# Performance work log

Measured on AMD Instinct MI355X. Metric: run time of the kernel, lower is better.

The kernel has to match this reference:

```python
import jax, jax.numpy as jnp
import numpy as np
import math

N_HEAD = 8

def setup_inputs() -> dict:
    key = jax.random.key(0)
    ks = jax.random.split(key, 5)
    B, T, D = 1, 4096, 512
    x = jax.random.normal(ks[0], (B, T, D), dtype=jnp.float32)
    s = 0.02
    Wq = jax.random.normal(ks[1], (D, D), dtype=jnp.float32) * s
    Wk = jax.random.normal(ks[2], (D, D), dtype=jnp.float32) * s
    Wv = jax.random.normal(ks[3], (D, D), dtype=jnp.float32) * s
    Wo = jax.random.normal(ks[4], (D, D), dtype=jnp.float32) * s
    return {"x": x, "Wq": Wq, "Wk": Wk, "Wv": Wv, "Wo": Wo, "window": 64}

def reference(x, Wq, Wk, Wv, Wo, window):
    # SparseAttention with attend_fn = causal sliding window of size `window`.
    # key_indices[q] = [max(0, q-window+1) .. q]
    B, T, D = x.shape
    H = N_HEAD
    Dh = D // H
    scale = math.sqrt(Dh)
    # torch Linear(bias=False): y = x @ W.T
    Q = (x @ Wq.T).reshape(B, T, H, Dh)
    K = (x @ Wk.T).reshape(B, T, H, Dh)
    V = (x @ Wv.T).reshape(B, T, H, Dh)
    # per-query gather indices [T, w] with validity mask (honors sparsity;
    # never materializes a [T, T] score matrix)
    offs = jnp.arange(window) - (window - 1)          # [-w+1 .. 0]
    idx = jnp.arange(T)[:, None] + offs[None, :]       # [T, w]
    valid = idx >= 0                                   # [T, w]
    idx_c = jnp.clip(idx, 0, T - 1)
    Kg = K[:, idx_c]                                   # [B, T, w, H, Dh]
    Vg = V[:, idx_c]                                   # [B, T, w, H, Dh]
    scores = jnp.einsum('bthd,btwhd->bhtw', Q, Kg) / scale
    scores = jnp.where(valid[None, None, :, :], scores, jnp.finfo(scores.dtype).min)
    attn = jax.nn.softmax(scores, axis=-1)             # dropout=0.0 (eval)
    out = jnp.einsum('bhtw,btwhd->bthd', attn, Vg).reshape(B, T, D)
    return out @ Wo.T
```

## Files before the change

kernel.cpp:

```cpp
#include <hip/hip_runtime.h>
#include <hip/hip_bf16.h>
#include <math.h>


typedef __attribute__((ext_vector_type(8))) short bf16frag;
typedef __attribute__((ext_vector_type(4))) float f32x4;
typedef __attribute__((ext_vector_type(8))) unsigned short u16x8;

#if defined(__has_builtin)
#if __has_builtin(__builtin_amdgcn_global_load_lds)
#define HAVE_GLOAD_LDS 1
#endif
#endif

__device__ inline void gload16(const void* g, void* l, int lane) {
#ifdef HAVE_GLOAD_LDS
    __builtin_amdgcn_global_load_lds(
        (const __attribute__((address_space(1))) void*)g,
        (__attribute__((address_space(3))) void*)l, 16, 0, 0);
#else
    *(bf16frag*)((char*)l + lane * 16) = *(const bf16frag*)g;
#endif
}

__device__ inline unsigned short bf16_rne(float f) {
    unsigned int u = __float_as_uint(f);
    unsigned int r = u + 0x7fffu + ((u >> 16) & 1u);
    return (unsigned short)(r >> 16);
}

__device__ inline void split_val(float f, unsigned short& h, unsigned short& l) {
    h = bf16_rne(f);
    float hf = __uint_as_float(((unsigned int)h) << 16);
    float lf = f - hf;
    l = bf16_rne(lf);
}

__global__ __launch_bounds__(256) void split5(
    const float* __restrict__ x, const float* __restrict__ wq, const float* __restrict__ wk,
    const float* __restrict__ wv, const float* __restrict__ wo,
    unsigned short* xh, unsigned short* xl, unsigned short* qh, unsigned short* ql,
    unsigned short* kh, unsigned short* kl, unsigned short* vh, unsigned short* vl,
    unsigned short* oh, unsigned short* ol, int nx, int nw)
{
    const float* src; unsigned short *H, *L; int n;
    switch (blockIdx.z) {
        case 0: src = x;  H = xh; L = xl; n = nx; break;
        case 1: src = wq; H = qh; L = ql; n = nw; break;
        case 2: src = wk; H = kh; L = kl; n = nw; break;
        case 3: src = wv; H = vh; L = vl; n = nw; break;
        default: src = wo; H = oh; L = ol; n = nw; break;
    }
    int stride = gridDim.x * blockDim.x * 4;
    for (int i = (blockIdx.x * blockDim.x + threadIdx.x) * 4; i < n; i += stride) {
        float4 f = *(const float4*)(src + i);
        ushort4 h4, l4;
        split_val(f.x, h4.x, l4.x);
        split_val(f.y, h4.y, l4.y);
        split_val(f.z, h4.z, l4.z);
        split_val(f.w, h4.w, l4.w);
        *(ushort4*)(H + i) = h4;
        *(ushort4*)(L + i) = l4;
    }
}

__global__ __launch_bounds__(256) void zero_pad(
    unsigned short* __restrict__ VTH, unsigned short* __restrict__ VTL, int vtw)
{
    int i = blockIdx.x * blockDim.x + threadIdx.x;
    if (i < 512 * 63) {
        int r = i / 63, c = i % 63;
        VTH[(size_t)r * vtw + c] = 0;
        VTL[(size_t)r * vtw + c] = 0;
    }
}

template<int BM, int MODE>
__global__ __launch_bounds__(256) void gemm_lds(
    const unsigned short* __restrict__ Ah, const unsigned short* __restrict__ Al,
    const unsigned short* __restrict__ W0h, const unsigned short* __restrict__ W0l,
    const unsigned short* __restrict__ W1h, const unsigned short* __restrict__ W1l,
    const unsigned short* __restrict__ W2h, const unsigned short* __restrict__ W2l,
    float* __restrict__ C0, float* __restrict__ C1, float* __restrict__ C2,
    unsigned short* __restrict__ QHo, unsigned short* __restrict__ QLo,
    unsigned short* __restrict__ KHo, unsigned short* __restrict__ KLo,
    unsigned short* __restrict__ VTHo, unsigned short* __restrict__ VTLo, int vtw)
{
    constexpr int MT     = BM / 32;
    constexpr int HALF   = BM / 2;
    constexpr int ABYTES = BM * 128;
    constexpr int NINST  = (BM + 64) * 128 / 1024;
    constexpr int PER_WAVE = NINST / 4;

    __shared__ unsigned char lds[(BM + 64) * 128];

    const unsigned short *Wh, *Wl;
    if (blockIdx.z == 0)      { Wh = W0h; Wl = W0l; }
    else if (blockIdx.z == 1) { Wh = W1h; Wl = W1l; }
    else                      { Wh = W2h; Wl = W2l; }

    const int tid  = threadIdx.x;
    const int wid  = tid >> 6;
    const int lane = tid & 63;
    const int wr = wid >> 1, wc = wid & 1;
    const int m0 = blockIdx.y * BM;
    const int n0 = blockIdx.x * 64;

    f32x4 acc[MT][2];
    #pragma unroll
    for (int i = 0; i < MT; ++i) {
        acc[i][0] = (f32x4){0.f, 0.f, 0.f, 0.f};
        acc[i][1] = (f32x4){0.f, 0.f, 0.f, 0.f};
    }

    for (int ks = 0; ks < 24; ++ks) {
        const int rg = ks >> 3;
        const int k0 = (ks & 7) << 6;
        const unsigned short* As = (rg < 2) ? Ah : Al;
        const unsigned short* Bs = (rg == 1) ? Wl : Wh;

        __syncthreads();
        #pragma unroll
        for (int j = 0; j < PER_WAVE; ++j) {
            const int o  = (wid * PER_WAVE + j) << 10;
            const int li = o + lane * 16;
            const void* g;
            if (li < ABYTES) {
                const int r  = li >> 7;
                const int kb = (li & 127) ^ ((r & 7) << 4);
                g = As + (size_t)(m0 + r) * 512 + k0 + (kb >> 1);
            } else {
                const int lb = li - ABYTES;
                const int r  = lb >> 7;
                const int kb = (lb & 127) ^ ((r & 7) << 4);
                g = Bs + (size_t)(n0 + r) * 512 + k0 + (kb >> 1);
            }
            gload16(g, lds + o, lane);
        }
        __syncthreads();

        #pragma unroll
        for (int ksub = 0; ksub < 2; ++ksub) {
            const int kbb = (ksub << 6) + ((lane >> 4) << 4);
            bf16frag af[MT], bf[2];
            #pragma unroll
            for (int mt = 0; mt < MT; ++mt) {
                const int r = wr * HALF + mt * 16 + (lane & 15);
                af[mt] = *(const bf16frag*)(lds + r * 128 + (kbb ^ ((r & 7) << 4)));
            }
            #pragma unroll
            for (int nt = 0; nt < 2; ++nt) {
                const int r = wc * 32 + nt * 16 + (lane & 15);
                bf[nt] = *(const bf16frag*)(lds + ABYTES + r * 128 + (kbb ^ ((r & 7) << 4)));
            }
            #pragma unroll
            for (int mt = 0; mt < MT; ++mt)
                #pragma unroll
                for (int nt = 0; nt < 2; ++nt)
                    acc[mt][nt] = __builtin_amdgcn_mfma_f32_16x16x32_bf16(
                        af[mt], bf[nt], acc[mt][nt], 0, 0, 0);
        }
    }

    const int rbase = (lane >> 4) * 4;
    #pragma unroll
    for (int mt = 0; mt < MT; ++mt)
        #pragma unroll
        for (int nt = 0; nt < 2; ++nt) {
            const int col = n0 + wc * 32 + nt * 16 + (lane & 15);
            #pragma unroll
            for (int j = 0; j < 4; ++j) {
                const int row = m0 + wr * HALF + mt * 16 + rbase + j;
                if constexpr (MODE == 0) {
                    float* C = (blockIdx.z == 0) ? C0 : (blockIdx.z == 1 ? C1 : C2);
                    C[(size_t)row * 512 + col] = acc[mt][nt][j];
                } else {
                    unsigned short hh, ll;
                    split_val(acc[mt][nt][j], hh, ll);
                    if (blockIdx.z == 0) {
                        QHo[(size_t)row * 512 + col] = hh;
                        QLo[(size_t)row * 512 + col] = ll;
                    } else if (blockIdx.z == 1) {
                        KHo[(size_t)row * 512 + col] = hh;
                        KLo[(size_t)row * 512 + col] = ll;
                    } else {
                        VTHo[(size_t)col * vtw + 63 + row] = hh;
                        VTLo[(size_t)col * vtw + 63 + row] = ll;
                    }
                }
            }
        }
}

__global__ __launch_bounds__(128) void swattn5(
    const unsigned short* __restrict__ QH, const unsigned short* __restrict__ QL,
    const unsigned short* __restrict__ KH, const unsigned short* __restrict__ KL,
    const unsigned short* __restrict__ VTH, const unsigned short* __restrict__ VTL,
    unsigned short* __restrict__ OH, unsigned short* __restrict__ OL, int T)
{
    __shared__ unsigned short KsH[96 * 88], KsL[96 * 88];
    __shared__ unsigned short VtH[64 * 104], VtL[64 * 104];
    __shared__ unsigned short PsH[32 * 104], PsL[32 * 104];

    const int h   = blockIdx.x & 7;
    const int t0  = (blockIdx.x >> 3) * 32;
    const int kt0 = t0 - 63;
    const int tid = threadIdx.x;
    const int vtw = T + 64;

    {
        const int c = tid & 7;
        for (int r = tid >> 3; r < 96; r += 16) {
            const int kt = kt0 + r;
            u16x8 kh = {0,0,0,0,0,0,0,0}, kl = {0,0,0,0,0,0,0,0};
            if (kt >= 0 && r < 95) {
                const size_t off = (size_t)kt * 512 + h * 64 + c * 8;
                kh = *(const u16x8*)(KH + off);
                kl = *(const u16x8*)(KL + off);
            }
            *(u16x8*)&KsH[r * 88 + c * 8] = kh;
            *(u16x8*)&KsL[r * 88 + c * 8] = kl;
        }
    }
    for (int i = tid; i < 64 * 12; i += 128) {
        const int d = i / 12, c = i % 12;
        const size_t off = (size_t)(h * 64 + d) * vtw + t0 + c * 8;
        *(u16x8*)&VtH[d * 104 + c * 8] = *(const u16x8*)(VTH + off);
        *(u16x8*)&VtL[d * 104 + c * 8] = *(const u16x8*)(VTL + off);
    }
    __syncthreads();

    const int wid  = tid >> 6;
    const int lane = tid & 63;
    const int lr = lane & 15;
    const int lg = lane >> 4;

    bf16frag qfh[2], qfl[2];
    {
        const size_t base = (size_t)(t0 + wid * 16 + lr) * 512 + h * 64 + lg * 8;
        qfh[0] = *(const bf16frag*)(QH + base);
        qfh[1] = *(const bf16frag*)(QH + base + 32);
        qfl[0] = *(const bf16frag*)(QL + base);
        qfl[1] = *(const bf16frag*)(QL + base + 32);
    }

    f32x4 s[6];
    #pragma unroll
    for (int wt = 0; wt < 6; ++wt) s[wt] = (f32x4){0.f, 0.f, 0.f, 0.f};
    #pragma unroll
    for (int ksub = 0; ksub < 2; ++ksub) {
        #pragma unroll
        for (int wt = 0; wt < 6; ++wt) {
            const int a = (wt * 16 + lr) * 88 + lg * 8 + ksub * 32;
            bf16frag akh = *(const bf16frag*)&KsH[a];
            bf16frag akl = *(const bf16frag*)&KsL[a];
            s[wt] = __builtin_amdgcn_mfma_f32_16x16x32_bf16(akh, qfh[ksub], s[wt], 0, 0, 0);
            s[wt] = __builtin_amdgcn_mfma_f32_16x16x32_bf16(akh, qfl[ksub], s[wt], 0, 0, 0);
            s[wt] = __builtin_amdgcn_mfma_f32_16x16x32_bf16(akl, qfh[ksub], s[wt], 0, 0, 0);
        }
    }

    const int q_local = wid * 16 + lr;
    float sc[6][4];
    float mx = -3e38f;
    #pragma unroll
    for (int wt = 0; wt < 6; ++wt)
        #pragma unroll
        for (int j = 0; j < 4; ++j) {
            const int w = wt * 16 + lg * 4 + j;
            const bool valid = (w >= q_local) && (w <= q_local + 63) && (kt0 + w >= 0);
            sc[wt][j] = valid ? s[wt][j] * 0.125f : -3e38f;
            mx = fmaxf(mx, sc[wt][j]);
        }
    mx = fmaxf(mx, __shfl_xor(mx, 16));
    mx = fmaxf(mx, __shfl_xor(mx, 32));
    float sum = 0.f;
    #pragma unroll
    for (int wt = 0; wt < 6; ++wt)
        #pragma unroll
        for (int j = 0; j < 4; ++j) {
            sc[wt][j] = __expf(sc[wt][j] - mx);
            sum += sc[wt][j];
        }
    sum += __shfl_xor(sum, 16);
    sum += __shfl_xor(sum, 32);
    const float inv = 1.f / sum;

    #pragma unroll
    for (int wt = 0; wt < 6; ++wt) {
        ushort4 ph, pl;
        unsigned short hh, ll;
        split_val(sc[wt][0] * inv, hh, ll); ph.x = hh; pl.x = ll;
        split_val(sc[wt][1] * inv, hh, ll); ph.y = hh; pl.y = ll;
        split_val(sc[wt][2] * inv, hh, ll); ph.z = hh; pl.z = ll;
        split_val(sc[wt][3] * inv, hh, ll); ph.w = hh; pl.w = ll;
        const int col = wt * 16 + lg * 4;
        *(ushort4*)&PsH[q_local * 104 + col] = ph;
        *(ushort4*)&PsL[q_local * 104 + col] = pl;
    }

    f32x4 oa[4];
    #pragma unroll
    for (int dt = 0; dt < 4; ++dt) oa[dt] = (f32x4){0.f, 0.f, 0.f, 0.f};
    #pragma unroll
    for (int ks = 0; ks < 3; ++ks) {
        const int ka = lg * 8 + ks * 32;
        bf16frag pah = *(const bf16frag*)&PsH[(wid * 16 + lr) * 104 + ka];
        bf16frag pal = *(const bf16frag*)&PsL[(wid * 16 + lr) * 104 + ka];
        #pragma unroll
        for (int dt = 0; dt < 4; ++dt) {
            const int a = (dt * 16 + lr) * 104 + ka;
            bf16frag bvh = *(const bf16frag*)&VtH[a];
            bf16frag bvl = *(const bf16frag*)&VtL[a];
            oa[dt] = __builtin_amdgcn_mfma_f32_16x16x32_bf16(pah, bvh, oa[dt], 0, 0, 0);
            oa[dt] = __builtin_amdgcn_mfma_f32_16x16x32_bf16(pal, bvh, oa[dt], 0, 0, 0);
            oa[dt] = __builtin_amdgcn_mfma_f32_16x16x32_bf16(pah, bvl, oa[dt], 0, 0, 0);
        }
    }

    #pragma unroll
    for (int dt = 0; dt < 4; ++dt) {
        const int d = dt * 16 + lr;
        #pragma unroll
        for (int j = 0; j < 4; ++j) {
            const int t = t0 + wid * 16 + lg * 4 + j;
            unsigned short hh, ll;
            split_val(oa[dt][j], hh, ll);
            const size_t oi = (size_t)t * 512 + h * 64 + d;
            OH[oi] = hh;
            OL[oi] = ll;
        }
    }
}

extern "C" void kernel_launch(void* const* d_in, const int* in_sizes, int n_in,
                              void* d_out, int out_size, void* d_ws, size_t ws_size,
                              hipStream_t stream) {
    const float* x  = (const float*)d_in[0];
    const float* Wq = (const float*)d_in[1];
    const float* Wk = (const float*)d_in[2];
    const float* Wv = (const float*)d_in[3];
    const float* Wo = (const float*)d_in[4];
    float* out = (float*)d_out;

    const int D = 512;
    const int T = in_sizes[0] / D;
    const size_t tdf = (size_t)T * D;
    const size_t wsz = (size_t)D * D;
    const int vtw = T + 64;
    const size_t vts = (size_t)D * vtw;

    unsigned short* qh  = (unsigned short*)d_ws;
    unsigned short* ql  = qh + tdf;
    unsigned short* kh  = ql + tdf;
    unsigned short* kl  = kh + tdf;
    unsigned short* vth = kl + tdf;
    unsigned short* vtl = vth + vts;
    unsigned short* abh = vtl + vts;
    unsigned short* abl = abh + tdf;
    unsigned short* xh  = abl + tdf;
    unsigned short* xl  = xh + tdf;
    unsigned short* wqh = xl + tdf;
    unsigned short* wql = wqh + wsz;
    unsigned short* wkh = wql + wsz;
    unsigned short* wkl = wkh + wsz;
    unsigned short* wvh = wkl + wsz;
    unsigned short* wvl = wvh + wsz;
    unsigned short* woh = wvl + wsz;
    unsigned short* wol = woh + wsz;

    dim3 blk(256);
    split5<<<dim3(256, 1, 5), blk, 0, stream>>>(
        x, Wq, Wk, Wv, Wo, xh, xl, wqh, wql, wkh, wkl, wvh, wvl, woh, wol,
        (int)tdf, (int)wsz);

    zero_pad<<<dim3((512 * 63 + 255) / 256), blk, 0, stream>>>(vth, vtl, vtw);

    gemm_lds<128, 1><<<dim3(D / 64, T / 128, 3), blk, 0, stream>>>(
        xh, xl, wqh, wql, wkh, wkl, wvh, wvl,
        nullptr, nullptr, nullptr,
        qh, ql, kh, kl, vth, vtl, vtw);

    swattn5<<<dim3(8 * T / 32), dim3(128), 0, stream>>>(
        qh, ql, kh, kl, vth, vtl, abh, abl, T);

    gemm_lds<64, 0><<<dim3(D / 64, T / 64, 1), blk, 0, stream>>>(
        abh, abl, woh, wol, woh, wol, woh, wol,
        out, out, out,
        nullptr, nullptr, nullptr, nullptr, nullptr, nullptr, 0);
}
```

Measured before the change: 146.2 us.

## Double-buffer LDS staging in GEMMs and compute V transposed as Wv·xᵀ

Both GEMM kernels now use two LDS buffers and prefetch the next K-slice while the current one is consumed, which drops one barrier per iteration and overlaps global loads with MFMA work. The V projection is recomputed as Wv times x-transpose, so the transposed V output is written with contiguous stores along T instead of strided column scatters. Q/K/V tiles go into one flat grid with computed tile assignment. This doubles LDS use per block, which may lower occupancy.

```diff
diff --git a/kernel.cpp b/kernel.cpp
--- a/kernel.cpp
+++ b/kernel.cpp
@@ -75,54 +75,65 @@
     }
 }
 
-template<int BM, int MODE>
-__global__ __launch_bounds__(256) void gemm_lds(
-    const unsigned short* __restrict__ Ah, const unsigned short* __restrict__ Al,
-    const unsigned short* __restrict__ W0h, const unsigned short* __restrict__ W0l,
-    const unsigned short* __restrict__ W1h, const unsigned short* __restrict__ W1l,
-    const unsigned short* __restrict__ W2h, const unsigned short* __restrict__ W2l,
-    float* __restrict__ C0, float* __restrict__ C1, float* __restrict__ C2,
+__global__ __launch_bounds__(256) void gemm_qkvt(
+    const unsigned short* __restrict__ xh, const unsigned short* __restrict__ xl,
+    const unsigned short* __restrict__ wqh, const unsigned short* __restrict__ wql,
+    const unsigned short* __restrict__ wkh, const unsigned short* __restrict__ wkl,
+    const unsigned short* __restrict__ wvh, const unsigned short* __restrict__ wvl,
     unsigned short* __restrict__ QHo, unsigned short* __restrict__ QLo,
     unsigned short* __restrict__ KHo, unsigned short* __restrict__ KLo,
-    unsigned short* __restrict__ VTHo, unsigned short* __restrict__ VTLo, int vtw)
+    unsigned short* __restrict__ VTH, unsigned short* __restrict__ VTL,
+    int T, int vtw)
 {
-    constexpr int MT     = BM / 32;
-    constexpr int HALF   = BM / 2;
-    constexpr int ABYTES = BM * 128;
-    constexpr int NINST  = (BM + 64) * 128 / 1024;
-    constexpr int PER_WAVE = NINST / 4;
-
-    __shared__ unsigned char lds[(BM + 64) * 128];
-
-    const unsigned short *Wh, *Wl;
-    if (blockIdx.z == 0)      { Wh = W0h; Wl = W0l; }
-    else if (blockIdx.z == 1) { Wh = W1h; Wl = W1l; }
-    else                      { Wh = W2h; Wl = W2l; }
+    constexpr int ABYTES = 128 * 128;
+    __shared__ unsigned char lds[2][(128 + 64) * 128];
 
     const int tid  = threadIdx.x;
     const int wid  = tid >> 6;
     const int lane = tid & 63;
     const int wr = wid >> 1, wc = wid & 1;
-    const int m0 = blockIdx.y * BM;
-    const int n0 = blockIdx.x * 64;
-
-    f32x4 acc[MT][2];
-    #pragma unroll
-    for (int i = 0; i < MT; ++i) {
+
+    const int NQK = 8 * (T / 128);
+    const int id  = blockIdx.x;
+    const unsigned short *Ah, *Al, *Bh, *Bl;
+    unsigned short *OH_, *OL_;
+    int m0, n0;
+    bool vt;
+    if (id < 2 * NQK) {
+        vt = false;
+        const int zq  = id / NQK;
+        const int rem = id % NQK;
+        n0 = (rem & 7) * 64;
+        m0 = (rem >> 3) * 128;
+        Ah = xh; Al = xl;
+        Bh = zq ? wkh : wqh;  Bl = zq ? wkl : wql;
+        OH_ = zq ? KHo : QHo; OL_ = zq ? KLo : QLo;
+    } else {
+        vt = true;
+        const int rem = id - 2 * NQK;
+        const int nx  = T / 64;
+        n0 = (rem % nx) * 64;
+        m0 = (rem / nx) * 128;
+        Ah = wvh; Al = wvl;
+        Bh = xh;  Bl = xl;
+        OH_ = VTH; OL_ = VTL;
+    }
+
+    f32x4 acc[4][2];
+    #pragma unroll
+    for (int i = 0; i < 4; ++i) {
         acc[i][0] = (f32x4){0.f, 0.f, 0.f, 0.f};
         acc[i][1] = (f32x4){0.f, 0.f, 0.f, 0.f};
     }
 
-    for (int ks = 0; ks < 24; ++ks) {
+    auto stage = [&](int buf, int ks) {
         const int rg = ks >> 3;
         const int k0 = (ks & 7) << 6;
         const unsigned short* As = (rg < 2) ? Ah : Al;
-        const unsigned short* Bs = (rg == 1) ? Wl : Wh;
-
-        __syncthreads();
-        #pragma unroll
-        for (int j = 0; j < PER_WAVE; ++j) {
-            const int o  = (wid * PER_WAVE + j) << 10;
+        const unsigned short* Bs = (rg == 1) ? Bl : Bh;
+        #pragma unroll
+        for (int j = 0; j < 6; ++j) {
+            const int o  = (wid * 6 + j) << 10;
             const int li = o + lane * 16;
             const void* g;
             if (li < ABYTES) {
@@ -135,59 +146,148 @@
                 const int kb = (lb & 127) ^ ((r & 7) << 4);
                 g = Bs + (size_t)(n0 + r) * 512 + k0 + (kb >> 1);
             }
-            gload16(g, lds + o, lane);
-        }
-        __syncthreads();
-
+            gload16(g, &lds[buf][o], lane);
+        }
+    };
+
+    stage(0, 0);
+    __syncthreads();
+    int cur = 0;
+    for (int ks = 0; ks < 24; ++ks) {
+        if (ks < 23) stage(cur ^ 1, ks + 1);
         #pragma unroll
         for (int ksub = 0; ksub < 2; ++ksub) {
             const int kbb = (ksub << 6) + ((lane >> 4) << 4);
-            bf16frag af[MT], bf[2];
-            #pragma unroll
-            for (int mt = 0; mt < MT; ++mt) {
-                const int r = wr * HALF + mt * 16 + (lane & 15);
-                af[mt] = *(const bf16frag*)(lds + r * 128 + (kbb ^ ((r & 7) << 4)));
+            bf16frag af[4], bf[2];
+            #pragma unroll
+            for (int mt = 0; mt < 4; ++mt) {
+                const int r = wr * 64 + mt * 16 + (lane & 15);
+                af[mt] = *(const bf16frag*)(&lds[cur][0] + r * 128 + (kbb ^ ((r & 7) << 4)));
             }
             #pragma unroll
             for (int nt = 0; nt < 2; ++nt) {
                 const int r = wc * 32 + nt * 16 + (lane & 15);
-                bf[nt] = *(const bf16frag*)(lds + ABYTES + r * 128 + (kbb ^ ((r & 7) << 4)));
-            }
-            #pragma unroll
-            for (int mt = 0; mt < MT; ++mt)
+                bf[nt] = *(const bf16frag*)(&lds[cur][0] + ABYTES + r * 128 + (kbb ^ ((r & 7) << 4)));
+            }
+            #pragma unroll
+            for (int mt = 0; mt < 4; ++mt)
                 #pragma unroll
                 for (int nt = 0; nt < 2; ++nt)
                     acc[mt][nt] = __builtin_amdgcn_mfma_f32_16x16x32_bf16(
                         af[mt], bf[nt], acc[mt][nt], 0, 0, 0);
         }
+        __syncthreads();
+        cur ^= 1;
     }
 
     const int rbase = (lane >> 4) * 4;
     #pragma unroll
-    for (int mt = 0; mt < MT; ++mt)
+    for (int mt = 0; mt < 4; ++mt)
         #pragma unroll
         for (int nt = 0; nt < 2; ++nt) {
             const int col = n0 + wc * 32 + nt * 16 + (lane & 15);
             #pragma unroll
             for (int j = 0; j < 4; ++j) {
-                const int row = m0 + wr * HALF + mt * 16 + rbase + j;
-                if constexpr (MODE == 0) {
-                    float* C = (blockIdx.z == 0) ? C0 : (blockIdx.z == 1 ? C1 : C2);
-                    C[(size_t)row * 512 + col] = acc[mt][nt][j];
+                const int row = m0 + wr * 64 + mt * 16 + rbase + j;
+                unsigned short hh, ll;
+                split_val(acc[mt][nt][j], hh, ll);
+                if (!vt) {
+                    OH_[(size_t)row * 512 + col] = hh;
+                    OL_[(size_t)row * 512 + col] = ll;
                 } else {
-                    unsigned short hh, ll;
-                    split_val(acc[mt][nt][j], hh, ll);
-                    if (blockIdx.z == 0) {
-                        QHo[(size_t)row * 512 + col] = hh;
-                        QLo[(size_t)row * 512 + col] = ll;
-                    } else if (blockIdx.z == 1) {
-                        KHo[(size_t)row * 512 + col] = hh;
-                        KLo[(size_t)row * 512 + col] = ll;
-                    } else {
-                        VTHo[(size_t)col * vtw + 63 + row] = hh;
-                        VTLo[(size_t)col * vtw + 63 + row] = ll;
-                    }
+                    OH_[(size_t)row * vtw + 63 + col] = hh;
+                    OL_[(size_t)row * vtw + 63 + col] = ll;
                 }
+            }
+        }
+}
+
+__global__ __launch_bounds__(256) void gemm_out(
+    const unsigned short* __restrict__ Ah, const unsigned short* __restrict__ Al,
+    const unsigned short* __restrict__ Wh, const unsigned short* __restrict__ Wl,
+    float* __restrict__ C)
+{
+    constexpr int ABYTES = 64 * 128;
+    __shared__ unsigned char lds[2][(64 + 64) * 128];
+
+    const int tid  = threadIdx.x;
+    const int wid  = tid >> 6;
+    const int lane = tid & 63;
+    const int wr = wid >> 1, wc = wid & 1;
+    const int m0 = blockIdx.y * 64;
+    const int n0 = blockIdx.x * 64;
+
+    f32x4 acc[2][2];
+    #pragma unroll
+    for (int i = 0; i < 2; ++i) {
+        acc[i][0] = (f32x4){0.f, 0.f, 0.f, 0.f};
+        acc[i][1] = (f32x4){0.f, 0.f, 0.f, 0.f};
+    }
+
+    auto stage = [&](int buf, int ks) {
+        const int rg = ks >> 3;
+        const int k0 = (ks & 7) << 6;
+        const unsigned short* As = (rg < 2) ? Ah : Al;
+        const unsigned short* Bs = (rg == 1) ? Wl : Wh;
+        #pragma unroll
+        for (int j = 0; j < 4; ++j) {
+            const int o  = (wid * 4 + j) << 10;
+            const int li = o + lane * 16;
+            const void* g;
+            if (li < ABYTES) {
+                const int r  = li >> 7;
+                const int kb = (li & 127) ^ ((r & 7) << 4);
+                g = As + (size_t)(m0 + r) * 512 + k0 + (kb >> 1);
+            } else {
+                const int lb = li - ABYTES;
+                const int r  = lb >> 7;
+                const int kb = (lb & 127) ^ ((r & 7) << 4);
+                g = Bs + (size_t)(n0 + r) * 512 + k0 + (kb >> 1);
+            }
+            gload16(g, &lds[buf][o], lane);
+        }
+    };
+
+    stage(0, 0);
+    __syncthreads();
+    int cur = 0;
+    for (int ks = 0; ks < 24; ++ks) {
+        if (ks < 23) stage(cur ^ 1, ks + 1);
+        #pragma unroll
+        for (int ksub = 0; ksub < 2; ++ksub) {
+            const int kbb = (ksub << 6) + ((lane >> 4) << 4);
+            bf16frag af[2], bf[2];
+            #pragma unroll
+            for (int mt = 0; mt < 2; ++mt) {
+                const int r = wr * 32 + mt * 16 + (lane & 15);
+                af[mt] = *(const bf16frag*)(&lds[cur][0] + r * 128 + (kbb ^ ((r & 7) << 4)));
+            }
+            #pragma unroll
+            for (int nt = 0; nt < 2; ++nt) {
+                const int r = wc * 32 + nt * 16 + (lane & 15);
+                bf[nt] = *(const bf16frag*)(&lds[cur][0] + ABYTES + r * 128 + (kbb ^ ((r & 7) << 4)));
+            }
+            #pragma unroll
+            for (int mt = 0; mt < 2; ++mt)
+                #pragma unroll
+                for (int nt = 0; nt < 2; ++nt)
+                    acc[mt][nt] = __builtin_amdgcn_mfma_f32_16x16x32_bf16(
+                        af[mt], bf[nt], acc[mt][nt], 0, 0, 0);
+        }
+        __syncthreads();
+        cur ^= 1;
+    }
+
+    const int rbase = (lane >> 4) * 4;
+    #pragma unroll
+    for (int mt = 0; mt < 2; ++mt)
+        #pragma unroll
+        for (int nt = 0; nt < 2; ++nt) {
+            const int col = n0 + wc * 32 + nt * 16 + (lane & 15);
+            #pragma unroll
+            for (int j = 0; j < 4; ++j) {
+                const int row = m0 + wr * 32 + mt * 16 + rbase + j;
+                C[(size_t)row * 512 + col] = acc[mt][nt][j];
             }
         }
 }
@@ -376,16 +476,15 @@
 
     zero_pad<<<dim3((512 * 63 + 255) / 256), blk, 0, stream>>>(vth, vtl, vtw);
 
-    gemm_lds<128, 1><<<dim3(D / 64, T / 128, 3), blk, 0, stream>>>(
+    const int NQK = 8 * (T / 128);
+    const int NVT = (T / 64) * (D / 128);
+    gemm_qkvt<<<dim3(2 * NQK + NVT), blk, 0, stream>>>(
         xh, xl, wqh, wql, wkh, wkl, wvh, wvl,
-        nullptr, nullptr, nullptr,
-        qh, ql, kh, kl, vth, vtl, vtw);
+        qh, ql, kh, kl, vth, vtl, T, vtw);
 
     swattn5<<<dim3(8 * T / 32), dim3(128), 0, stream>>>(
         qh, ql, kh, kl, vth, vtl, abh, abl, T);
 
-    gemm_lds<64, 0><<<dim3(D / 64, T / 64, 1), blk, 0, stream>>>(
-        abh, abl, woh, wol, woh, wol, woh, wol,
-        out, out, out,
-        nullptr, nullptr, nullptr, nullptr, nullptr, nullptr, 0);
-}
+    gemm_out<<<dim3(D / 64, T / 64), blk, 0, stream>>>(
+        abh, abl, woh, wol, out);
+}
```

Result: faster. 140.4 us (-4.0%).
